# Performance work log

Measured on AMD Instinct MI355X. Metric: run time of the kernel, lower is better.

The kernel has to match this reference:

```python
import jax, jax.numpy as jnp
import numpy as np
from jax import lax

B = 512        # batch
SPEC = 300     # spectral bands / num_patches
DIM = 64
DEPTH = 5
HEADS = 4
DIM_HEAD = 16
MLP = 8
NCLS = 16
SCALE = DIM_HEAD ** -0.5


def setup_inputs() -> dict:
    key = jax.random.key(0)
    ks = jax.random.split(key, 16)
    s = 0.02
    d = {}
    d["input_tensor"] = jax.random.normal(ks[0], (B, 1, 5, 5, SPEC), jnp.float32)
    # SSE block: Conv3d(1,1,(1,1,300)) == contraction over spectral dim
    d["sse_w"] = jax.random.normal(ks[1], (SPEC,), jnp.float32) * s
    d["sse_b"] = jnp.zeros((1,), jnp.float32)
    # 3D CNN branch
    d["conv1_w"] = jax.random.normal(ks[2], (16, 1, 3, 3, 7), jnp.float32) * s
    d["conv1_b"] = jnp.zeros((16,), jnp.float32)
    d["conv2_w"] = jax.random.normal(ks[3], (32, 16, 3, 3, 3), jnp.float32) * s
    d["conv2_b"] = jnp.zeros((32,), jnp.float32)
    d["dense1_w"] = jax.random.normal(ks[4], (64, 9344), jnp.float32) * s
    d["dense1_b"] = jnp.zeros((64,), jnp.float32)
    # patch embedding + tokens
    d["patch_w"] = jax.random.normal(ks[5], (DIM, 25), jnp.float32) * s
    d["patch_b"] = jnp.zeros((DIM,), jnp.float32)
    d["cls_token"] = jax.random.normal(ks[6], (1, 1, DIM), jnp.float32)
    d["pos_emb"] = jax.random.normal(ks[7], (1, SPEC + 1, DIM), jnp.float32)
    # transformer layers (stacked over depth)
    d["ln1_g"] = jnp.ones((DEPTH, DIM), jnp.float32)
    d["ln1_b"] = jnp.zeros((DEPTH, DIM), jnp.float32)
    d["qkv_w"] = jax.random.normal(ks[8], (DEPTH, 3 * HEADS * DIM_HEAD, DIM), jnp.float32) * s
    d["attn_out_w"] = jax.random.normal(ks[9], (DEPTH, DIM, HEADS * DIM_HEAD), jnp.float32) * s
    d["attn_out_b"] = jnp.zeros((DEPTH, DIM), jnp.float32)
    d["ln2_g"] = jnp.ones((DEPTH, DIM), jnp.float32)
    d["ln2_b"] = jnp.zeros((DEPTH, DIM), jnp.float32)
    d["ff1_w"] = jax.random.normal(ks[10], (DEPTH, MLP, DIM), jnp.float32) * s
    d["ff1_b"] = jnp.zeros((DEPTH, MLP), jnp.float32)
    d["ff2_w"] = jax.random.normal(ks[11], (DEPTH, DIM, MLP), jnp.float32) * s
    d["ff2_b"] = jnp.zeros((DEPTH, DIM), jnp.float32)
    # head: LayerNorm(2*dim) + Linear(2*dim, num_classes)
    d["head_ln_g"] = jnp.ones((2 * DIM,), jnp.float32)
    d["head_ln_b"] = jnp.zeros((2 * DIM,), jnp.float32)
    d["head_w"] = jax.random.normal(ks[12], (NCLS, 2 * DIM), jnp.float32) * s
    d["head_b"] = jnp.zeros((NCLS,), jnp.float32)
    return d


def _ln(x, g, b, eps=1e-5):
    m = jnp.mean(x, -1, keepdims=True)
    v = jnp.mean((x - m) ** 2, -1, keepdims=True)
    return (x - m) * lax.rsqrt(v + eps) * g + b


def reference(input_tensor, sse_w, sse_b, conv1_w, conv1_b, conv2_w, conv2_b,
              dense1_w, dense1_b, patch_w, patch_b, cls_token, pos_emb,
              ln1_g, ln1_b, qkv_w, attn_out_w, attn_out_b, ln2_g, ln2_b,
              ff1_w, ff1_b, ff2_w, ff2_b, head_ln_g, head_ln_b, head_w, head_b):
    xin = input_tensor  # [B,1,5,5,300]
    # Spatial SE: Conv3d(1,1,(1,1,300)) -> sigmoid -> gate
    sq = jax.nn.sigmoid(jnp.einsum('bihwc,c->bhw', xin, sse_w)[:, None, :, :, None] + sse_b[0])
    xin = xin * sq

    # ---- 3D CNN branch ----
    dn = ('NCDHW', 'OIDHW', 'NCDHW')
    h = lax.conv_general_dilated(xin, conv1_w, (1, 1, 1), 'VALID', dimension_numbers=dn)
    h = jax.nn.relu(h + conv1_b[None, :, None, None, None])          # [B,16,3,3,294]
    h = lax.conv_general_dilated(h, conv2_w, (1, 1, 1), 'VALID', dimension_numbers=dn)
    h = jax.nn.relu(h + conv2_b[None, :, None, None, None])          # [B,32,1,1,292]
    y = h.reshape(h.shape[0], -1) @ dense1_w.T + dense1_b            # [B,64]

    # ---- SpectralFormer branch ----
    b = xin.shape[0]
    # torch .view(b, 1*300, 5*5) on contiguous [B,1,5,5,300]: pure C-order reshape
    x = xin.reshape(b, SPEC, 25)
    x = x @ patch_w.T + patch_b                                      # [B,300,64]
    cls = jnp.broadcast_to(cls_token, (b, 1, DIM))
    x = jnp.concatenate([cls, x], axis=1) + pos_emb[:, :SPEC + 1]    # [B,301,64]

    for i in range(DEPTH):
        # attention (residual + prenorm)
        xn = _ln(x, ln1_g[i], ln1_b[i])
        qkv = xn @ qkv_w[i].T                                        # [B,301,192]
        q, k, v = jnp.split(qkv, 3, axis=-1)
        def heads(t):
            return t.reshape(b, SPEC + 1, HEADS, DIM_HEAD).transpose(0, 2, 1, 3)
        q, k, v = heads(q), heads(k), heads(v)                       # [B,H,301,16]
        dots = jnp.einsum('bhid,bhjd->bhij', q, k) * SCALE
        attn = jax.nn.softmax(dots, axis=-1)
        o = jnp.einsum('bhij,bhjd->bhid', attn, v)
        o = o.transpose(0, 2, 1, 3).reshape(b, SPEC + 1, HEADS * DIM_HEAD)
        x = o @ attn_out_w[i].T + attn_out_b[i] + x
        # feedforward (residual + prenorm)
        xn = _ln(x, ln2_g[i], ln2_b[i])
        hid = jax.nn.gelu(xn @ ff1_w[i].T + ff1_b[i], approximate=False)
        x = hid @ ff2_w[i].T + ff2_b[i] + x

    cls_out = x[:, 0]                                                # [B,64]
    z = jnp.concatenate([cls_out, y], axis=-1)                       # [B,128]
    z = _ln(z, head_ln_g, head_ln_b)
    return z @ head_w.T + head_b                                     # [B,16]
```

## Files before the change

### kernel.cpp

```cpp
#include <hip/hip_runtime.h>
#include <cmath>

#define NB 512
#define SEQ 301
#define QSCALE 0.36067376022f

using f32x4  = __attribute__((ext_vector_type(4))) float;
using s16x4  = __attribute__((ext_vector_type(4))) short;
using s16x8  = __attribute__((ext_vector_type(8))) short;

#if __has_builtin(__builtin_amdgcn_exp2f)
#define EX2(x) __builtin_amdgcn_exp2f(x)
#else
#define EX2(x) exp2f(x)
#endif

__device__ __forceinline__ unsigned short f2bf(float f) {
  unsigned int u = __builtin_bit_cast(unsigned int, f);
  u += 0x7fffu + ((u >> 16) & 1u);
  return (unsigned short)(u >> 16);
}

__device__ __forceinline__ unsigned int pkbf(float lo, float hi) {
  unsigned int ulo = __builtin_bit_cast(unsigned int, lo) + 0x8000u;
  unsigned int uhi = __builtin_bit_cast(unsigned int, hi) + 0x8000u;
  return __builtin_amdgcn_perm(uhi, ulo, 0x07060302u);
}

__device__ __forceinline__ s16x4 pk4f(float a, float b, float c, float d) {
  uint2 u = make_uint2(pkbf(a, b), pkbf(c, d));
  return __builtin_bit_cast(s16x4, u);
}

__device__ __forceinline__ s16x4 pk4(float4 v) {
  return pk4f(v.x, v.y, v.z, v.w);
}

__device__ __forceinline__ f32x4 mm16(s16x4 a, s16x4 b, f32x4 c) {
  return __builtin_amdgcn_mfma_f32_16x16x16bf16_1k(a, b, c, 0, 0, 0);
}

__device__ __forceinline__ f32x4 mm32(s16x8 a, s16x8 b, f32x4 c) {
  return __builtin_amdgcn_mfma_f32_16x16x32_bf16(a, b, c, 0, 0, 0);
}

__device__ __forceinline__ s16x8 cat8(s16x4 a, s16x4 b) {
  return __builtin_shufflevector(a, b, 0, 1, 2, 3, 4, 5, 6, 7);
}

__device__ __forceinline__ float gelu_f(float a) {
  float z = fabsf(a) * 0.70710678f;
  float t = 1.f / (1.f + 0.3275911f * z);
  float poly = t*(0.254829592f + t*(-0.284496736f + t*(1.421413741f +
               t*(-1.453152027f + t*1.061405429f))));
  float e = EX2(-z*z*1.44269504f);
  float erfa = 1.f - poly*e;
  float erfz = copysignf(erfa, a);
  return 0.5f*a*(1.f + erfz);
}

__global__ __launch_bounds__(256) void k_prep(const float* __restrict__ w2c,
    unsigned short* __restrict__ wt2g) {
  int i = blockIdx.x*256 + threadIdx.x;
  if (i >= 96*148) return;
  int row = i/148, k = i - row*148;
  int kw_ = row >> 5, o2 = row & 31;
  unsigned short v = 0;
  if (k < 144) {
    int ci = k/9, r_ = k - ci*9;
    v = f2bf(w2c[o2*432 + ci*27 + r_*3 + kw_]);
  }
  wt2g[i] = v;
}

__global__ __launch_bounds__(256) void k_prep2(const float* __restrict__ pw,
    unsigned short* __restrict__ pwt) {
  int i = blockIdx.x*256 + threadIdx.x;
  if (i >= 64*32) return;
  int d = i >> 5, k = i & 31;
  pwt[i] = (k < 25) ? f2bf(pw[d*25 + k]) : (unsigned short)0;
}

__global__ __launch_bounds__(64) void k_sse(const float* __restrict__ xin,
    const float* __restrict__ sw, const float* __restrict__ sb, float* __restrict__ xs) {
  int blk = blockIdx.x; int b = blk / 25, p = blk % 25; int lane = threadIdx.x;
  const float* src = xin + (size_t)b*7500 + p*300;
  float s = 0.f;
  for (int c = lane; c < 300; c += 64) s += src[c]*sw[c];
  #pragma unroll
  for (int o = 32; o > 0; o >>= 1) s += __shfl_down(s, o, 64);
  s = __shfl(s, 0, 64);
  float sq = 1.f/(1.f + __expf(-(s + sb[0])));
  float* dst = xs + (size_t)b*7500 + p*300;
  for (int c = lane; c < 300; c += 64) dst[c] = src[c]*sq;
}

__global__ __launch_bounds__(256) void k_conv12(const float* __restrict__ xs,
    const float* __restrict__ w1c, const float* __restrict__ b1c,
    const unsigned short* __restrict__ wt2g, const float* __restrict__ b2c,
    float* __restrict__ c2) {
  int blk = blockIdx.x; int b = blk >> 2; int chunk = blk & 3;
  int w0 = chunk*73;
  int tid = threadIdx.x;
  int lane = tid & 63, wv = tid >> 6;
  int lm = lane & 15, lq = lane >> 4;
  __shared__ unsigned short xss[32*88];
  __shared__ unsigned short c1s[84*148];
  __shared__ alignas(8) unsigned short wt_s[96*148];

  const float* src = xs + (size_t)b*7500;
  for (int i = tid; i < 2025; i += 256) {
    int p = i/81, c = i - p*81;
    xss[p*88 + c] = f2bf(src[p*300 + w0 + c]);
  }
  for (int i = tid; i < 7*88; i += 256) xss[25*88 + i] = 0;
  for (int i = tid; i < 25*7; i += 256) { int p = i/7, c = 81 + i%7; xss[p*88 + c] = 0; }
  for (int i = tid; i < 9*148; i += 256) c1s[75*148 + i] = 0;
  {
    const uint2* wsrc = (const uint2*)wt2g;
    uint2* wdst = (uint2*)wt_s;
    for (int i = tid; i < 3552; i += 256) wdst[i] = wsrc[i];
  }

  s16x4 Af[4]; int P[4][4]; float bv[4];
  #pragma unroll
  for (int r = 0; r < 4; ++r) bv[r] = b1c[lq*4 + r];
  #pragma unroll
  for (int kc = 0; kc < 4; ++kc) {
    short e[4];
    #pragma unroll
    for (int j = 0; j < 4; ++j) {
      int k = kc*16 + lq*4 + j;
      float wf = (k < 63) ? w1c[lm*63 + k] : 0.f;
      e[j] = (short)f2bf(wf);
      int r_ = k/7, kw_ = k - r_*7;
      int kd = r_/3, kh = r_ - kd*3;
      P[kc][j] = (kd*5 + kh)*88 + kw_;
    }
    s16x4 a; a.x = e[0]; a.y = e[1]; a.z = e[2]; a.w = e[3];
    Af[kc] = a;
  }
  __syncthreads();

  for (int idx = wv; idx < 45; idx += 4) {
    int dh = idx/5, pt = idx - dh*5;
    int d0 = dh/3, h0 = dh - d0*3;
    int base = (d0*5 + h0)*88 + pt*16 + lm;
    f32x4 acc = {bv[0], bv[1], bv[2], bv[3]};
    #pragma unroll
    for (int kc = 0; kc < 4; ++kc) {
      s16x4 Bf;
      Bf.x = (short)xss[base + P[kc][0]];
      Bf.y = (short)xss[base + P[kc][1]];
      Bf.z = (short)xss[base + P[kc][2]];
      Bf.w = (short)xss[base + P[kc][3]];
      acc = mm16(Af[kc], Bf, acc);
    }
    int lw = pt*16 + lm;
    if (lw < 75) {
      unsigned short* dst = c1s + lw*148 + dh;
      #pragma unroll
      for (int r = 0; r < 4; ++r)
        dst[(lq*4 + r)*9] = f2bf(fmaxf(acc[r], 0.f));
    }
  }
  __syncthreads();

  float bvo0 = b2c[lm], bvo1 = b2c[16 + lm];
  for (int task = wv; task < 10; task += 4) {
    int pt = task >> 1, ot = task & 1;
    float bb = ot ? bvo1 : bvo0;
    f32x4 acc = {bb, bb, bb, bb};
    #pragma unroll
    for (int kw_ = 0; kw_ < 3; ++kw_) {
      int rowb = (pt*16 + lm + kw_)*148;
      int wrow = (kw_*32 + ot*16 + lm)*148;
      #pragma unroll
      for (int kc = 0; kc < 9; ++kc) {
        s16x4 Aw = *(const s16x4*)&c1s[rowb + kc*16 + lq*4];
        s16x4 Bw = *(const s16x4*)&wt_s[wrow + kc*16 + lq*4];
        acc = mm16(Aw, Bw, acc);
      }
    }
    float* dst = c2 + (size_t)b*9344 + (ot*16 + lm)*292;
    #pragma unroll
    for (int r = 0; r < 4; ++r) {
      int w2l = pt*16 + lq*4 + r;
      if (w2l < 73) dst[w0 + w2l] = fmaxf(acc[r], 0.f);
    }
  }
}

__global__ __launch_bounds__(256) void k_dense1(const float* __restrict__ c2,
    const float* __restrict__ w, float* __restrict__ part) {
  int mt = blockIdx.x & 31;
  int kc = blockIdx.x >> 5;
  int b0 = mt * 16;
  int tid = threadIdx.x;
  int lane = tid & 63; int nt = tid >> 6;
  int lm = lane & 15, lq = lane >> 4;
  int s0 = kc*36 + (kc < 8 ? kc : 8);
  int cnt = 36 + (kc < 8 ? 1 : 0);
  const float* arow = c2 + (size_t)(b0 + lm)*9344;
  const float* brow = w + (size_t)(nt*16 + lm)*9344;
  f32x4 acc = {0.f, 0.f, 0.f, 0.f};
  int koff = s0*16 + lq*4;
  #pragma unroll 4
  for (int i = 0; i < cnt; ++i, koff += 16) {
    s16x4 af = pk4(*(const float4*)(arow + koff));
    s16x4 bf = pk4(*(const float4*)(brow + koff));
    acc = mm16(af, bf, acc);
  }
  float* dst = part + (size_t)kc*32768;
  #pragma unroll
  for (int r = 0; r < 4; ++r)
    dst[(size_t)(b0 + lq*4 + r)*64 + nt*16 + lm] = acc[r];
}

__global__ __launch_bounds__(256) void k_patch(const float* __restrict__ xs,
    const unsigned short* __restrict__ pwt, const float* __restrict__ pb,
    const float* __restrict__ cls, const float* __restrict__ pos, float* __restrict__ x) {
  int b = blockIdx.x;
  int tid = threadIdx.x;
  int lane = tid & 63; int nt = tid >> 6;
  int lm = lane & 15, lq = lane >> 4;
  __shared__ unsigned short P_s[304*36];

  const float* src = xs + (size_t)b*7500;
  for (int i = tid; i < 304*32; i += 256) {
    int row = i >> 5, k = i & 31;
    unsigned short v = 0;
    if (row >= 1 && row <= 300 && k < 25) v = f2bf(src[(row-1)*25 + k]);
    P_s[row*36 + k] = v;
  }
  __syncthreads();

  int d = nt*16 + lm;
  s16x4 Bf0 = *(const s16x4*)&pwt[d*32 + lq*4];
  s16x4 Bf1 = *(const s16x4*)&pwt[d*32 + 16 + lq*4];
  float pbd = pb[d];
  float clsd = cls[d];
  for (int rt = 0; rt < 19; ++rt) {
    const unsigned short* prow = &P_s[(rt*16 + lm)*36];
    s16x4 A0 = *(const s16x4*)&prow[lq*4];
    s16x4 A1 = *(const s16x4*)&prow[16 + lq*4];
    f32x4 acc = {0.f,0.f,0.f,0.f};
    acc = mm16(A0, Bf0, acc);
    acc = mm16(A1, Bf1, acc);
    #pragma unroll
    for (int r = 0; r < 4; ++r) {
      int t = rt*16 + lq*4 + r;
      if (t < SEQ) {
        float val = acc[r] + pbd + pos[t*64 + d];
        if (t == 0) val = clsd + pos[d];
        x[((size_t)b*SEQ + t)*64 + d] = val;
      }
    }
  }
}

__global__ __launch_bounds__(256) void k_attn(const float* __restrict__ x,
    const float* __restrict__ g, const float* __restrict__ bt,
    const float* __restrict__ qkvw, unsigned short* __restrict__ ao) {
  int b = blockIdx.x;
  int tid = threadIdx.x;
  int lane = tid & 63, h = tid >> 6;
  int lm = lane & 15, lq = lane >> 4;
  __shared__ unsigned short xn_s[304*68];

  for (int rr = tid; rr < 304; rr += 256) {
    int src = rr < 301 ? rr : 300;
    const float4* xp = (const float4*)(x + ((size_t)b*SEQ + src)*64);
    float4 xv[16];
    #pragma unroll
    for (int i = 0; i < 16; ++i) xv[i] = xp[i];
    float m = 0.f;
    #pragma unroll
    for (int i = 0; i < 16; ++i) m += xv[i].x + xv[i].y + xv[i].z + xv[i].w;
    m *= (1.f/64.f);
    float var = 0.f;
    #pragma unroll
    for (int i = 0; i < 16; ++i) {
      float a = xv[i].x-m, bb = xv[i].y-m, c = xv[i].z-m, dd = xv[i].w-m;
      var += a*a + bb*bb + c*c + dd*dd;
    }
    float rs = rsqrtf(var*(1.f/64.f) + 1e-5f);
    const float4* g4 = (const float4*)g;
    const float4* b4 = (const float4*)bt;
    #pragma unroll
    for (int i = 0; i < 16; ++i) {
      float4 gg = g4[i]; float4 bb = b4[i];
      float e0 = (xv[i].x-m)*rs*gg.x + bb.x;
      float e1 = (xv[i].y-m)*rs*gg.y + bb.y;
      float e2 = (xv[i].z-m)*rs*gg.z + bb.z;
      float e3 = (xv[i].w-m)*rs*gg.w + bb.w;
      *(uint2*)&xn_s[rr*68 + i*4] = make_uint2(pkbf(e0, e1), pkbf(e2, e3));
    }
  }

  s16x4 WqA[4], WkA[4], WvB[4];
  #pragma unroll
  for (int c = 0; c < 4; ++c) {
    float4 wq = *(const float4*)(qkvw + (size_t)(h*16 + lm)*64 + c*16 + lq*4);
    WqA[c] = pk4f(wq.x*QSCALE, wq.y*QSCALE, wq.z*QSCALE, wq.w*QSCALE);
    WkA[c] = pk4(*(const float4*)(qkvw + (size_t)(64 + h*16 + lm)*64 + c*16 + lq*4));
    WvB[c] = pk4(*(const float4*)(qkvw + (size_t)(128 + h*16 + lm)*64 + c*16 + lq*4));
  }
  __syncthreads();

  s16x4 Kreg[19], Vreg[19];
  #pragma unroll
  for (int rt = 0; rt < 19; ++rt) {
    s16x4 Af[4];
    #pragma unroll
    for (int c = 0; c < 4; ++c)
      Af[c] = *(const s16x4*)&xn_s[(rt*16 + lm)*68 + c*16 + lq*4];
    f32x4 aK = {0.f,0.f,0.f,0.f}, aV = {0.f,0.f,0.f,0.f};
    #pragma unroll
    for (int c = 0; c < 4; ++c) {
      aK = mm16(WkA[c], Af[c], aK);
      aV = mm16(Af[c], WvB[c], aV);
    }
    Kreg[rt] = pk4f(aK[0], aK[1], aK[2], aK[3]);
    Vreg[rt] = pk4f(aV[0], aV[1], aV[2], aV[3]);
  }

  for (int pi = 0; pi < 10; ++pi) {
    int qt0 = 2*pi;
    int qt1 = 2*pi + 1;
    bool two = (qt1 < 19);
    int qt1c = two ? qt1 : qt0;
    s16x4 qb0, qb1;
    {
      s16x4 Af0[4], Af1[4];
      #pragma unroll
      for (int c = 0; c < 4; ++c) {
        Af0[c] = *(const s16x4*)&xn_s[(qt0*16 + lm)*68 + c*16 + lq*4];
        Af1[c] = *(const s16x4*)&xn_s[(qt1c*16 + lm)*68 + c*16 + lq*4];
      }
      f32x4 a0 = {0.f,0.f,0.f,0.f}, a1 = {0.f,0.f,0.f,0.f};
      #pragma unroll
      for (int c = 0; c < 4; ++c) {
        a0 = mm16(WqA[c], Af0[c], a0);
        a1 = mm16(WqA[c], Af1[c], a1);
      }
      qb0 = pk4f(a0[0], a0[1], a0[2], a0[3]);
      qb1 = pk4f(a1[0], a1[1], a1[2], a1[3]);
    }
    f32x4 o0 = {0.f,0.f,0.f,0.f}, o1 = {0.f,0.f,0.f,0.f};
    float l0 = 0.f, l1 = 0.f;
    #pragma unroll
    for (int t = 0; t < 9; ++t) {
      s16x4 kaa = Kreg[2*t];
      s16x4 kab = Kreg[2*t + 1];
      s16x8 vb = cat8(Vreg[2*t], Vreg[2*t + 1]);
      f32x4 z = {0.f,0.f,0.f,0.f};
      f32x4 s0a = mm16(kaa, qb0, z);
      f32x4 s0b = mm16(kab, qb0, z);
      f32x4 s1a = mm16(kaa, qb1, z);
      f32x4 s1b = mm16(kab, qb1, z);
      float p00 = EX2(s0a[0]), p01 = EX2(s0a[1]), p02 = EX2(s0a[2]), p03 = EX2(s0a[3]);
      float p04 = EX2(s0b[0]), p05 = EX2(s0b[1]), p06 = EX2(s0b[2]), p07 = EX2(s0b[3]);
      float p10 = EX2(s1a[0]), p11 = EX2(s1a[1]), p12 = EX2(s1a[2]), p13 = EX2(s1a[3]);
      float p14 = EX2(s1b[0]), p15 = EX2(s1b[1]), p16 = EX2(s1b[2]), p17 = EX2(s1b[3]);
      l0 += ((p00 + p01) + (p02 + p03)) + ((p04 + p05) + (p06 + p07));
      l1 += ((p10 + p11) + (p12 + p13)) + ((p14 + p15) + (p16 + p17));
      s16x8 pa0 = cat8(pk4f(p00, p01, p02, p03), pk4f(p04, p05, p06, p07));
      s16x8 pa1 = cat8(pk4f(p10, p11, p12, p13), pk4f(p14, p15, p16, p17));
      o0 = mm32(pa0, vb, o0);
      o1 = mm32(pa1, vb, o1);
    }
    {
      s16x4 ka = Kreg[18];
      s16x4 vb = Vreg[18];
      f32x4 z = {0.f,0.f,0.f,0.f};
      f32x4 st0 = mm16(ka, qb0, z);
      f32x4 st1 = mm16(ka, qb1, z);
      int kbase = 288 + lq*4;
      float p00 = (kbase + 0 < SEQ) ? EX2(st0[0]) : 0.f;
      float p01 = (kbase + 1 < SEQ) ? EX2(st0[1]) : 0.f;
      float p02 = (kbase + 2 < SEQ) ? EX2(st0[2]) : 0.f;
      float p03 = (kbase + 3 < SEQ) ? EX2(st0[3]) : 0.f;
      float p10 = (kbase + 0 < SEQ) ? EX2(st1[0]) : 0.f;
      float p11 = (kbase + 1 < SEQ) ? EX2(st1[1]) : 0.f;
      float p12 = (kbase + 2 < SEQ) ? EX2(st1[2]) : 0.f;
      float p13 = (kbase + 3 < SEQ) ? EX2(st1[3]) : 0.f;
      l0 += (p00 + p01) + (p02 + p03);
      l1 += (p10 + p11) + (p12 + p13);
      s16x4 pa0 = pk4f(p00, p01, p02, p03);
      s16x4 pa1 = pk4f(p10, p11, p12, p13);
      o0 = mm16(pa0, vb, o0);
      o1 = mm16(pa1, vb, o1);
    }
    l0 += __shfl_xor(l0, 16, 64); l0 += __shfl_xor(l0, 32, 64);
    l1 += __shfl_xor(l1, 16, 64); l1 += __shfl_xor(l1, 32, 64);
    float li0 = 1.f / l0;
    float li1 = 1.f / l1;
    #pragma unroll
    for (int r = 0; r < 4; ++r) {
      int q0 = qt0*16 + lq*4 + r;
      float lr0 = __shfl(li0, lq*4 + r, 64);
      if (q0 < SEQ) ao[((size_t)b*SEQ + q0)*64 + h*16 + lm] = f2bf(o0[r] * lr0);
      if (two) {
        int q1 = qt1*16 + lq*4 + r;
        float lr1 = __shfl(li1, lq*4 + r, 64);
        if (q1 < SEQ) ao[((size_t)b*SEQ + q1)*64 + h*16 + lm] = f2bf(o1[r] * lr1);
      }
    }
  }
}

__global__ __launch_bounds__(64) void k_post(const unsigned short* __restrict__ ao,
    const float* __restrict__ w, const float* __restrict__ bias,
    const float* __restrict__ g, const float* __restrict__ bt,
    const float* __restrict__ w1, const float* __restrict__ b1,
    const float* __restrict__ w2, const float* __restrict__ b2,
    float* __restrict__ x) {
  int b = blockIdx.x >> 3; int w0 = blockIdx.x & 7;
  int lane = threadIdx.x;
  int lm = lane & 15, lq = lane >> 4;

  s16x4 Bf[4][4];
  #pragma unroll
  for (int nt = 0; nt < 4; ++nt) {
    #pragma unroll
    for (int c = 0; c < 4; ++c) {
      float4 wf = *(const float4*)(w + (size_t)(nt*16 + lm)*64 + c*16 + lq*4);
      Bf[nt][c] = pk4(wf);
    }
  }
  float biasv[4], gv[4], btv[4], b2v[4];
  float w1r[8][4], w2r[4][8];
  float b1v[8];
  #pragma unroll
  for (int nt = 0; nt < 4; ++nt) {
    biasv[nt] = bias[nt*16 + lm];
    gv[nt]    = g[nt*16 + lm];
    btv[nt]   = bt[nt*16 + lm];
    b2v[nt]   = b2[nt*16 + lm];
    #pragma unroll
    for (int t = 0; t < 8; ++t) w2r[nt][t] = w2[(nt*16 + lm)*8 + t];
  }
  #pragma unroll
  for (int t = 0; t < 8; ++t) {
    b1v[t] = b1[t];
    #pragma unroll
    for (int nt = 0; nt < 4; ++nt) w1r[t][nt] = w1[t*64 + nt*16 + lm];
  }

  for (int rt = w0; rt < 19; rt += 8) {
    int rsrc = rt*16 + lm; if (rsrc > 300) rsrc = 300;
    const unsigned short* arow = ao + ((size_t)b*SEQ + rsrc)*64;
    int row0 = rt*16 + lq*4;
    float xpre[4][4];
    #pragma unroll
    for (int r = 0; r < 4; ++r) {
      int row = row0 + r; int rs2 = row > 300 ? 300 : row;
      const float* xr = x + ((size_t)b*SEQ + rs2)*64;
      #pragma unroll
      for (int nt = 0; nt < 4; ++nt) xpre[r][nt] = xr[nt*16 + lm];
    }
    f32x4 acc[4];
    #pragma unroll
    for (int nt = 0; nt < 4; ++nt)
      acc[nt] = (f32x4){biasv[nt], biasv[nt], biasv[nt], biasv[nt]};
    #pragma unroll
    for (int c = 0; c < 4; ++c) {
      s16x4 af = *(const s16x4*)(arow + c*16 + lq*4);
      #pragma unroll
      for (int nt = 0; nt < 4; ++nt) acc[nt] = mm16(af, Bf[nt][c], acc[nt]);
    }
    float v[4][4];
    #pragma unroll
    for (int r = 0; r < 4; ++r)
      #pragma unroll
      for (int nt = 0; nt < 4; ++nt) v[r][nt] = acc[nt][r] + xpre[r][nt];
    #pragma unroll
    for (int r = 0; r < 4; ++r) {
      float s = (v[r][0] + v[r][1]) + (v[r][2] + v[r][3]);
      s += __shfl_xor(s, 1, 64); s += __shfl_xor(s, 2, 64);
      s += __shfl_xor(s, 4, 64); s += __shfl_xor(s, 8, 64);
      float m = s * (1.f/64.f);
      float c0 = v[r][0]-m, c1 = v[r][1]-m, c2 = v[r][2]-m, c3 = v[r][3]-m;
      float s2 = (c0*c0 + c1*c1) + (c2*c2 + c3*c3);
      s2 += __shfl_xor(s2, 1, 64); s2 += __shfl_xor(s2, 2, 64);
      s2 += __shfl_xor(s2, 4, 64); s2 += __shfl_xor(s2, 8, 64);
      float rs = rsqrtf(s2*(1.f/64.f) + 1e-5f);
      float xn0 = c0*rs*gv[0] + btv[0];
      float xn1 = c1*rs*gv[1] + btv[1];
      float xn2 = c2*rs*gv[2] + btv[2];
      float xn3 = c3*rs*gv[3] + btv[3];
      float hg[8];
      #pragma unroll
      for (int t = 0; t < 8; ++t) {
        float p = xn0*w1r[t][0] + xn1*w1r[t][1] + xn2*w1r[t][2] + xn3*w1r[t][3];
        p += __shfl_xor(p, 1, 64); p += __shfl_xor(p, 2, 64);
        p += __shfl_xor(p, 4, 64); p += __shfl_xor(p, 8, 64);
        hg[t] = gelu_f(p + b1v[t]);
      }
      int row = row0 + r;
      if (row < SEQ) {
        float* xw = x + ((size_t)b*SEQ + row)*64;
        #pragma unroll
        for (int nt = 0; nt < 4; ++nt) {
          float o = 0.f;
          #pragma unroll
          for (int t = 0; t < 8; ++t) o += hg[t]*w2r[nt][t];
          xw[nt*16 + lm] = v[r][nt] + o + b2v[nt];
        }
      }
    }
  }
}

__global__ __launch_bounds__(128) void k_head(const float* __restrict__ x,
    const float* __restrict__ part, const float* __restrict__ d1b,
    const float* __restrict__ g, const float* __restrict__ bt,
    const float* __restrict__ hw, const float* __restrict__ hb, float* __restrict__ out) {
  int b = blockIdx.x; int t = threadIdx.x; int lane = t & 63; int wv = t >> 6;
  float v;
  if (t < 64) {
    v = x[(size_t)b*SEQ*64 + t];
  } else {
    int o = t - 64;
    float acc = d1b[o];
    #pragma unroll
    for (int kc = 0; kc < 16; ++kc) acc += part[(size_t)kc*32768 + b*64 + o];
    v = acc;
  }
  __shared__ float rbuf[2];
  __shared__ float z_s[128];
  float s = v;
  #pragma unroll
  for (int o = 32; o; o >>= 1) s += __shfl_down(s, o, 64);
  if (lane == 0) rbuf[wv] = s;
  __syncthreads();
  float m = (rbuf[0] + rbuf[1]) * (1.f/128.f);
  __syncthreads();
  float c = v - m;
  float s2 = c*c;
  #pragma unroll
  for (int o = 32; o; o >>= 1) s2 += __shfl_down(s2, o, 64);
  if (lane == 0) rbuf[wv] = s2;
  __syncthreads();
  float var = (rbuf[0] + rbuf[1]) * (1.f/128.f);
  z_s[t] = c * rsqrtf(var + 1e-5f) * g[t] + bt[t];
  __syncthreads();
  if (t < 16) {
    float a = hb[t];
    const float* wr = hw + t*128;
    #pragma unroll 8
    for (int j = 0; j < 128; ++j) a += z_s[j]*wr[j];
    out[(size_t)b*16 + t] = a;
  }
}

extern "C" void kernel_launch(void* const* d_in, const int* in_sizes, int n_in,
                              void* d_out, int out_size, void* d_ws, size_t ws_size,
                              hipStream_t stream) {
  const float* input      = (const float*)d_in[0];
  const float* sse_w      = (const float*)d_in[1];
  const float* sse_b      = (const float*)d_in[2];
  const float* conv1_w    = (const float*)d_in[3];
  const float* conv1_b    = (const float*)d_in[4];
  const float* conv2_w    = (const float*)d_in[5];
  const float* conv2_b    = (const float*)d_in[6];
  const float* dense1_w   = (const float*)d_in[7];
  const float* dense1_b   = (const float*)d_in[8];
  const float* patch_w    = (const float*)d_in[9];
  const float* patch_b    = (const float*)d_in[10];
  const float* cls_token  = (const float*)d_in[11];
  const float* pos_emb    = (const float*)d_in[12];
  const float* ln1_g      = (const float*)d_in[13];
  const float* ln1_b      = (const float*)d_in[14];
  const float* qkv_w      = (const float*)d_in[15];
  const float* attn_out_w = (const float*)d_in[16];
  const float* attn_out_b = (const float*)d_in[17];
  const float* ln2_g      = (const float*)d_in[18];
  const float* ln2_b      = (const float*)d_in[19];
  const float* ff1_w      = (const float*)d_in[20];
  const float* ff1_b      = (const float*)d_in[21];
  const float* ff2_w      = (const float*)d_in[22];
  const float* ff2_b      = (const float*)d_in[23];
  const float* head_ln_g  = (const float*)d_in[24];
  const float* head_ln_b  = (const float*)d_in[25];
  const float* head_w     = (const float*)d_in[26];
  const float* head_b     = (const float*)d_in[27];
  float* out = (float*)d_out;

  float* ws = (float*)d_ws;
  float* xs  = ws;
  float* part = ws;
  float* y   = xs + 3840000;
  unsigned short* wt2g = (unsigned short*)y;
  unsigned short* pwt  = (unsigned short*)(y + 16384);
  float* x   = y + 32768;
  float* R   = x + 9863168;
  float* c2  = R + 21676032;
  unsigned short* ao = (unsigned short*)R;

  k_prep  <<<56, 256, 0, stream>>>(conv2_w, wt2g);
  k_prep2 <<<8, 256, 0, stream>>>(patch_w, pwt);
  k_sse   <<<NB*25, 64, 0, stream>>>(input, sse_w, sse_b, xs);
  k_conv12<<<NB*4, 256, 0, stream>>>(xs, conv1_w, conv1_b, wt2g, conv2_b, c2);
  k_patch <<<NB, 256, 0, stream>>>(xs, pwt, patch_b, cls_token, pos_emb, x);
  k_dense1<<<512, 256, 0, stream>>>(c2, dense1_w, part);
  for (int i = 0; i < 5; ++i) {
    k_attn<<<NB, 256, 0, stream>>>(x, ln1_g + i*64, ln1_b + i*64,
                                   qkv_w + (size_t)i*192*64, ao);
    k_post<<<NB*8, 64, 0, stream>>>(ao,
                 attn_out_w + (size_t)i*4096, attn_out_b + i*64,
                 ln2_g + i*64, ln2_b + i*64,
                 ff1_w + (size_t)i*512, ff1_b + i*8, ff2_w + (size_t)i*512, ff2_b + i*64, x);
  }
  k_head<<<NB, 128, 0, stream>>>(x, part, dense1_b, head_ln_g, head_ln_b, head_w, head_b, out);
}
```

Measured before the change: 749.7 us.

## Fuse attention and post-attention MLP kernels into one per-layer kernel

Merges the attention kernel and the output-projection/LayerNorm/FFN kernel into a single per-batch kernel separated by a block barrier. The goal is to remove one launch per layer and let the attention output be reread while still cached. In exchange, the post phase now uses 4 waves per batch instead of 8 separate blocks. The combined kernel may also raise register pressure and lower occupancy.

```diff
diff --git a/kernel.cpp b/kernel.cpp
--- a/kernel.cpp
+++ b/kernel.cpp
@@ -259,9 +259,13 @@
   }
 }
 
-__global__ __launch_bounds__(256) void k_attn(const float* __restrict__ x,
+__global__ __launch_bounds__(256) void k_layer(float* __restrict__ x,
     const float* __restrict__ g, const float* __restrict__ bt,
-    const float* __restrict__ qkvw, unsigned short* __restrict__ ao) {
+    const float* __restrict__ qkvw, unsigned short* __restrict__ ao,
+    const float* __restrict__ w, const float* __restrict__ bias,
+    const float* __restrict__ g2, const float* __restrict__ bt2,
+    const float* __restrict__ w1, const float* __restrict__ b1,
+    const float* __restrict__ w2, const float* __restrict__ b2) {
   int b = blockIdx.x;
   int tid = threadIdx.x;
   int lane = tid & 63, h = tid >> 6;
@@ -408,105 +412,100 @@
       }
     }
   }
-}
-
-__global__ __launch_bounds__(64) void k_post(const unsigned short* __restrict__ ao,
-    const float* __restrict__ w, const float* __restrict__ bias,
-    const float* __restrict__ g, const float* __restrict__ bt,
-    const float* __restrict__ w1, const float* __restrict__ b1,
-    const float* __restrict__ w2, const float* __restrict__ b2,
-    float* __restrict__ x) {
-  int b = blockIdx.x >> 3; int w0 = blockIdx.x & 7;
-  int lane = threadIdx.x;
-  int lm = lane & 15, lq = lane >> 4;
-
-  s16x4 Bf[4][4];
-  #pragma unroll
-  for (int nt = 0; nt < 4; ++nt) {
-    #pragma unroll
-    for (int c = 0; c < 4; ++c) {
-      float4 wf = *(const float4*)(w + (size_t)(nt*16 + lm)*64 + c*16 + lq*4);
-      Bf[nt][c] = pk4(wf);
-    }
-  }
-  float biasv[4], gv[4], btv[4], b2v[4];
-  float w1r[8][4], w2r[4][8];
-  float b1v[8];
-  #pragma unroll
-  for (int nt = 0; nt < 4; ++nt) {
-    biasv[nt] = bias[nt*16 + lm];
-    gv[nt]    = g[nt*16 + lm];
-    btv[nt]   = bt[nt*16 + lm];
-    b2v[nt]   = b2[nt*16 + lm];
-    #pragma unroll
-    for (int t = 0; t < 8; ++t) w2r[nt][t] = w2[(nt*16 + lm)*8 + t];
-  }
-  #pragma unroll
-  for (int t = 0; t < 8; ++t) {
-    b1v[t] = b1[t];
-    #pragma unroll
-    for (int nt = 0; nt < 4; ++nt) w1r[t][nt] = w1[t*64 + nt*16 + lm];
-  }
-
-  for (int rt = w0; rt < 19; rt += 8) {
-    int rsrc = rt*16 + lm; if (rsrc > 300) rsrc = 300;
-    const unsigned short* arow = ao + ((size_t)b*SEQ + rsrc)*64;
-    int row0 = rt*16 + lq*4;
-    float xpre[4][4];
-    #pragma unroll
-    for (int r = 0; r < 4; ++r) {
-      int row = row0 + r; int rs2 = row > 300 ? 300 : row;
-      const float* xr = x + ((size_t)b*SEQ + rs2)*64;
-      #pragma unroll
-      for (int nt = 0; nt < 4; ++nt) xpre[r][nt] = xr[nt*16 + lm];
-    }
-    f32x4 acc[4];
-    #pragma unroll
-    for (int nt = 0; nt < 4; ++nt)
-      acc[nt] = (f32x4){biasv[nt], biasv[nt], biasv[nt], biasv[nt]};
-    #pragma unroll
-    for (int c = 0; c < 4; ++c) {
-      s16x4 af = *(const s16x4*)(arow + c*16 + lq*4);
-      #pragma unroll
-      for (int nt = 0; nt < 4; ++nt) acc[nt] = mm16(af, Bf[nt][c], acc[nt]);
-    }
-    float v[4][4];
-    #pragma unroll
-    for (int r = 0; r < 4; ++r)
-      #pragma unroll
-      for (int nt = 0; nt < 4; ++nt) v[r][nt] = acc[nt][r] + xpre[r][nt];
-    #pragma unroll
-    for (int r = 0; r < 4; ++r) {
-      float s = (v[r][0] + v[r][1]) + (v[r][2] + v[r][3]);
-      s += __shfl_xor(s, 1, 64); s += __shfl_xor(s, 2, 64);
-      s += __shfl_xor(s, 4, 64); s += __shfl_xor(s, 8, 64);
-      float m = s * (1.f/64.f);
-      float c0 = v[r][0]-m, c1 = v[r][1]-m, c2 = v[r][2]-m, c3 = v[r][3]-m;
-      float s2 = (c0*c0 + c1*c1) + (c2*c2 + c3*c3);
-      s2 += __shfl_xor(s2, 1, 64); s2 += __shfl_xor(s2, 2, 64);
-      s2 += __shfl_xor(s2, 4, 64); s2 += __shfl_xor(s2, 8, 64);
-      float rs = rsqrtf(s2*(1.f/64.f) + 1e-5f);
-      float xn0 = c0*rs*gv[0] + btv[0];
-      float xn1 = c1*rs*gv[1] + btv[1];
-      float xn2 = c2*rs*gv[2] + btv[2];
-      float xn3 = c3*rs*gv[3] + btv[3];
-      float hg[8];
-      #pragma unroll
-      for (int t = 0; t < 8; ++t) {
-        float p = xn0*w1r[t][0] + xn1*w1r[t][1] + xn2*w1r[t][2] + xn3*w1r[t][3];
-        p += __shfl_xor(p, 1, 64); p += __shfl_xor(p, 2, 64);
-        p += __shfl_xor(p, 4, 64); p += __shfl_xor(p, 8, 64);
-        hg[t] = gelu_f(p + b1v[t]);
-      }
-      int row = row0 + r;
-      if (row < SEQ) {
-        float* xw = x + ((size_t)b*SEQ + row)*64;
+  __syncthreads();
+#if __has_builtin(__builtin_amdgcn_sched_barrier)
+  __builtin_amdgcn_sched_barrier(0);
+#endif
+
+  {
+    s16x4 Bf[4][4];
+    #pragma unroll
+    for (int nt = 0; nt < 4; ++nt) {
+      #pragma unroll
+      for (int c = 0; c < 4; ++c) {
+        float4 wf = *(const float4*)(w + (size_t)(nt*16 + lm)*64 + c*16 + lq*4);
+        Bf[nt][c] = pk4(wf);
+      }
+    }
+    float biasv[4], gv[4], btv[4], b2v[4];
+    float w1r[8][4], w2r[4][8];
+    float b1v[8];
+    #pragma unroll
+    for (int nt = 0; nt < 4; ++nt) {
+      biasv[nt] = bias[nt*16 + lm];
+      gv[nt]    = g2[nt*16 + lm];
+      btv[nt]   = bt2[nt*16 + lm];
+      b2v[nt]   = b2[nt*16 + lm];
+      #pragma unroll
+      for (int t = 0; t < 8; ++t) w2r[nt][t] = w2[(nt*16 + lm)*8 + t];
+    }
+    #pragma unroll
+    for (int t = 0; t < 8; ++t) {
+      b1v[t] = b1[t];
+      #pragma unroll
+      for (int nt = 0; nt < 4; ++nt) w1r[t][nt] = w1[t*64 + nt*16 + lm];
+    }
+
+    for (int rt = h; rt < 19; rt += 4) {
+      int rsrc = rt*16 + lm; if (rsrc > 300) rsrc = 300;
+      const unsigned short* arow = ao + ((size_t)b*SEQ + rsrc)*64;
+      int row0 = rt*16 + lq*4;
+      float xpre[4][4];
+      #pragma unroll
+      for (int r = 0; r < 4; ++r) {
+        int row = row0 + r; int rs2 = row > 300 ? 300 : row;
+        const float* xr = x + ((size_t)b*SEQ + rs2)*64;
         #pragma unroll
-        for (int nt = 0; nt < 4; ++nt) {
-          float o = 0.f;
+        for (int nt = 0; nt < 4; ++nt) xpre[r][nt] = xr[nt*16 + lm];
+      }
+      f32x4 acc[4];
+      #pragma unroll
+      for (int nt = 0; nt < 4; ++nt)
+        acc[nt] = (f32x4){biasv[nt], biasv[nt], biasv[nt], biasv[nt]};
+      #pragma unroll
+      for (int c = 0; c < 4; ++c) {
+        s16x4 af = *(const s16x4*)(arow + c*16 + lq*4);
+        #pragma unroll
+        for (int nt = 0; nt < 4; ++nt) acc[nt] = mm16(af, Bf[nt][c], acc[nt]);
+      }
+      float v[4][4];
+      #pragma unroll
+      for (int r = 0; r < 4; ++r)
+        #pragma unroll
+        for (int nt = 0; nt < 4; ++nt) v[r][nt] = acc[nt][r] + xpre[r][nt];
+      #pragma unroll
+      for (int r = 0; r < 4; ++r) {
+        float s = (v[r][0] + v[r][1]) + (v[r][2] + v[r][3]);
+        s += __shfl_xor(s, 1, 64); s += __shfl_xor(s, 2, 64);
+        s += __shfl_xor(s, 4, 64); s += __shfl_xor(s, 8, 64);
+        float m = s * (1.f/64.f);
+        float c0 = v[r][0]-m, c1 = v[r][1]-m, c2 = v[r][2]-m, c3 = v[r][3]-m;
+        float s2 = (c0*c0 + c1*c1) + (c2*c2 + c3*c3);
+        s2 += __shfl_xor(s2, 1, 64); s2 += __shfl_xor(s2, 2, 64);
+        s2 += __shfl_xor(s2, 4, 64); s2 += __shfl_xor(s2, 8, 64);
+        float rs = rsqrtf(s2*(1.f/64.f) + 1e-5f);
+        float xn0 = c0*rs*gv[0] + btv[0];
+        float xn1 = c1*rs*gv[1] + btv[1];
+        float xn2 = c2*rs*gv[2] + btv[2];
+        float xn3 = c3*rs*gv[3] + btv[3];
+        float hg[8];
+        #pragma unroll
+        for (int t = 0; t < 8; ++t) {
+          float p = xn0*w1r[t][0] + xn1*w1r[t][1] + xn2*w1r[t][2] + xn3*w1r[t][3];
+          p += __shfl_xor(p, 1, 64); p += __shfl_xor(p, 2, 64);
+          p += __shfl_xor(p, 4, 64); p += __shfl_xor(p, 8, 64);
+          hg[t] = gelu_f(p + b1v[t]);
+        }
+        int row = row0 + r;
+        if (row < SEQ) {
+          float* xw = x + ((size_t)b*SEQ + row)*64;
           #pragma unroll
-          for (int t = 0; t < 8; ++t) o += hg[t]*w2r[nt][t];
-          xw[nt*16 + lm] = v[r][nt] + o + b2v[nt];
+          for (int nt = 0; nt < 4; ++nt) {
+            float o = 0.f;
+            #pragma unroll
+            for (int t = 0; t < 8; ++t) o += hg[t]*w2r[nt][t];
+            xw[nt*16 + lm] = v[r][nt] + o + b2v[nt];
+          }
         }
       }
     }
@@ -606,12 +605,11 @@
   k_patch <<<NB, 256, 0, stream>>>(xs, pwt, patch_b, cls_token, pos_emb, x);
   k_dense1<<<512, 256, 0, stream>>>(c2, dense1_w, part);
   for (int i = 0; i < 5; ++i) {
-    k_attn<<<NB, 256, 0, stream>>>(x, ln1_g + i*64, ln1_b + i*64,
-                                   qkv_w + (size_t)i*192*64, ao);
-    k_post<<<NB*8, 64, 0, stream>>>(ao,
+    k_layer<<<NB, 256, 0, stream>>>(x, ln1_g + i*64, ln1_b + i*64,
+                 qkv_w + (size_t)i*192*64, ao,
                  attn_out_w + (size_t)i*4096, attn_out_b + i*64,
                  ln2_g + i*64, ln2_b + i*64,
-                 ff1_w + (size_t)i*512, ff1_b + i*8, ff2_w + (size_t)i*512, ff2_b + i*64, x);
+                 ff1_w + (size_t)i*512, ff1_b + i*8, ff2_w + (size_t)i*512, ff2_b + i*64);
   }
   k_head<<<NB, 128, 0, stream>>>(x, part, dense1_b, head_ln_g, head_ln_b, head_w, head_b, out);
 }
```

After: 664.8 us. 11.3% less time.
